# Performance work log

Hardware: AMD Instinct MI355X
Metric: run time of the kernel (lower is better)

Reference implementation:

```python
import jax, jax.numpy as jnp
import numpy as np

B, S, D, H, DK = 8, 1024, 1024, 16, 64
DV = D // H  # 64


def setup_inputs() -> dict:
    key = jax.random.key(0)
    ks = jax.random.split(key, 9)
    s = 1.0 / np.sqrt(D)
    return {
        "x": jax.random.normal(ks[0], (B, S, D), dtype=jnp.float32),
        "masks": jnp.ones((B, S), dtype=jnp.int32),
        "Wq": jax.random.normal(ks[1], (D, H * DK), dtype=jnp.float32) * s,
        "bq": jnp.zeros((H * DK,), dtype=jnp.float32),
        "Wk": jax.random.normal(ks[2], (D, H * DK), dtype=jnp.float32) * s,
        "bk": jnp.zeros((H * DK,), dtype=jnp.float32),
        "Wv": jax.random.normal(ks[3], (D, H * DV), dtype=jnp.float32) * s,
        "bv": jnp.zeros((H * DV,), dtype=jnp.float32),
        "Wo": jax.random.normal(ks[4], (H * DV, D), dtype=jnp.float32) * s,
        "bo": jnpp_zeros() if False else jnp.zeros((D,), dtype=jnp.float32),
    }


def reference(x, masks, Wq, bq, Wk, bk, Wv, bv, Wo, bo):
    # projections -> [B, H, S, d]
    q = (x @ Wq + bq).reshape(B, S, H, DK).transpose(0, 2, 1, 3)
    k = (x @ Wk + bk).reshape(B, S, H, DK).transpose(0, 2, 1, 3)
    v = (x @ Wv + bv).reshape(B, S, H, DV).transpose(0, 2, 1, 3)
    # scaled dot-product attention with padding mask
    logits = jnp.einsum('bhqd,bhkd->bhqk', q, k) / jnp.sqrt(jnp.float32(DK))
    mask = masks[:, None, None, :]  # [B,1,1,S]
    logits = jnp.where(mask == 0, jnp.float32(-1e9), logits)
    scores = jax.nn.softmax(logits, axis=-1)
    out = jnp.einsum('bhqk,bhkd->bhqd', scores, v)
    out = out.transpose(0, 2, 1, 3).reshape(B, S, H * DV)
    # output projection; dropout is identity in eval mode
    return out @ Wo + bo
```

## Files before the change

### kernel.cpp

```cpp
#include <hip/hip_runtime.h>
#include <stdint.h>

#define B_ 8
#define S_ 1024
#define D_ 1024
#define H_ 16
#define DK_ 64
#define DV_ 64

typedef __attribute__((ext_vector_type(8))) short short8;
typedef __attribute__((ext_vector_type(4))) float f32x4;

__device__ __forceinline__ unsigned short f2bf(float f) {
  union { float f; unsigned u; } v; v.f = f;
  return (unsigned short)((v.u + 0x7fffu + ((v.u >> 16) & 1u)) >> 16);
}
__device__ __forceinline__ unsigned short f2bf_trunc(float f) {
  union { float f; unsigned u; } v; v.f = f;
  return (unsigned short)(v.u >> 16);
}

__device__ __forceinline__ void ld_lds16(const unsigned short* g, unsigned short* l) {
  __builtin_amdgcn_global_load_lds((const __attribute__((address_space(1))) void*)g,
                                   (__attribute__((address_space(3))) void*)l, 16, 0, 0);
}

__global__ __launch_bounds__(256) void prep_kernel(const float* __restrict__ x,
                                                   unsigned short* __restrict__ xb,
                                                   const float* __restrict__ W0,
                                                   const float* __restrict__ W1,
                                                   const float* __restrict__ W2,
                                                   const float* __restrict__ W3,
                                                   unsigned short* __restrict__ T0,
                                                   unsigned short* __restrict__ T1,
                                                   unsigned short* __restrict__ T2,
                                                   unsigned short* __restrict__ T3) {
  const int z = blockIdx.z;
  if (z >= 4) {
    size_t blk = (size_t)(z - 4) * 256 + blockIdx.y * 16 + blockIdx.x;
    size_t i = (blk * 256 + threadIdx.x) * 4;
    float4 v = *(const float4*)(x + i);
    ushort4 o;
    o.x = f2bf(v.x); o.y = f2bf(v.y); o.z = f2bf(v.z); o.w = f2bf(v.w);
    *(ushort4*)(xb + i) = o;
    return;
  }
  __shared__ __align__(16) unsigned short tl[64][65];
  const float* W; unsigned short* Wt;
  switch (z) {
    case 0: W = W0; Wt = T0; break;
    case 1: W = W1; Wt = T1; break;
    case 2: W = W2; Wt = T2; break;
    default: W = W3; Wt = T3; break;
  }
  const int xx = threadIdx.x & 63;
  const int y4 = threadIdx.x >> 6;
  const int bn = blockIdx.x * 64;
  const int bk = blockIdx.y * 64;
  #pragma unroll
  for (int r = y4; r < 64; r += 4)
    tl[r][xx] = f2bf(W[(size_t)(bk + r) * 1024 + bn + xx]);
  __syncthreads();
  #pragma unroll
  for (int r = y4; r < 64; r += 4)
    Wt[(size_t)(bn + r) * 1024 + bk + xx] = tl[xx][r];
}


struct SJob { const unsigned short* g; unsigned short* l; };

__device__ __forceinline__ void stage128(const unsigned short* __restrict__ G,
                                         unsigned short* __restrict__ L, int t) {
  #pragma unroll
  for (int i = 0; i < 2; i++) {
    int s = i * 512 + t;
    int r = s >> 3, cb = s & 7;
    int c = cb ^ (r & 7);
    ld_lds16(G + (size_t)r * 1024 + c * 8, L + (size_t)s * 8);
  }
}

template <bool SW>
__device__ __forceinline__ f32x4 MM(short8 a, short8 b, f32x4 c) {
  if constexpr (SW) return __builtin_amdgcn_mfma_f32_16x16x32_bf16(b, a, c, 0, 0, 0);
  else              return __builtin_amdgcn_mfma_f32_16x16x32_bf16(a, b, c, 0, 0, 0);
}

template <bool SW, int VM>
__device__ __forceinline__ void ktile(const unsigned short* __restrict__ As_,
                                      const unsigned short* __restrict__ Bs_,
                                      f32x4 (&acc)[4][4],
                                      SJob s0, SJob s1, SJob s2,
                                      int t, int wm, int wn, int l15, int quad, int l7) {
  const int cb0 = (quad ^ l7) * 8;
  const int cb1 = ((4 | quad) ^ l7) * 8;
  short8 b0[4], b1[4];

  short8 a0k0 = *(const short8*)&As_[(wm + 0 * 16 + l15) * 64 + cb0];
  short8 a1k0 = *(const short8*)&As_[(wm + 1 * 16 + l15) * 64 + cb0];
  #pragma unroll
  for (int ni = 0; ni < 4; ni++)
    b0[ni] = *(const short8*)&Bs_[(wn + ni * 16 + l15) * 64 + cb0];
  if (s0.g) stage128(s0.g, s0.l, t);
  __builtin_amdgcn_s_barrier();
  asm volatile("s_waitcnt lgkmcnt(0)" ::: "memory");
  __builtin_amdgcn_s_setprio(1);
  #pragma unroll
  for (int ni = 0; ni < 4; ni++) {
    acc[0][ni] = MM<SW>(a0k0, b0[ni], acc[0][ni]);
    acc[1][ni] = MM<SW>(a1k0, b0[ni], acc[1][ni]);
  }
  __builtin_amdgcn_s_setprio(0);
  __builtin_amdgcn_s_barrier();

  short8 a0k1 = *(const short8*)&As_[(wm + 0 * 16 + l15) * 64 + cb1];
  short8 a1k1 = *(const short8*)&As_[(wm + 1 * 16 + l15) * 64 + cb1];
  #pragma unroll
  for (int ni = 0; ni < 4; ni++)
    b1[ni] = *(const short8*)&Bs_[(wn + ni * 16 + l15) * 64 + cb1];
  if (s1.g) stage128(s1.g, s1.l, t);
  __builtin_amdgcn_s_barrier();
  asm volatile("s_waitcnt lgkmcnt(0)" ::: "memory");
  __builtin_amdgcn_s_setprio(1);
  #pragma unroll
  for (int ni = 0; ni < 4; ni++) {
    acc[0][ni] = MM<SW>(a0k1, b1[ni], acc[0][ni]);
    acc[1][ni] = MM<SW>(a1k1, b1[ni], acc[1][ni]);
  }
  __builtin_amdgcn_s_setprio(0);
  __builtin_amdgcn_s_barrier();

  short8 a2k0 = *(const short8*)&As_[(wm + 2 * 16 + l15) * 64 + cb0];
  short8 a3k0 = *(const short8*)&As_[(wm + 3 * 16 + l15) * 64 + cb0];
  if (s2.g) stage128(s2.g, s2.l, t);
  __builtin_amdgcn_s_barrier();
  asm volatile("s_waitcnt lgkmcnt(0)" ::: "memory");
  __builtin_amdgcn_s_setprio(1);
  #pragma unroll
  for (int ni = 0; ni < 4; ni++) {
    acc[2][ni] = MM<SW>(a2k0, b0[ni], acc[2][ni]);
    acc[3][ni] = MM<SW>(a3k0, b0[ni], acc[3][ni]);
  }
  __builtin_amdgcn_s_setprio(0);
  __builtin_amdgcn_s_barrier();

  short8 a2k1 = *(const short8*)&As_[(wm + 2 * 16 + l15) * 64 + cb1];
  short8 a3k1 = *(const short8*)&As_[(wm + 3 * 16 + l15) * 64 + cb1];
  __builtin_amdgcn_s_barrier();
  asm volatile("s_waitcnt lgkmcnt(0)" ::: "memory");
  __builtin_amdgcn_s_setprio(1);
  #pragma unroll
  for (int ni = 0; ni < 4; ni++) {
    acc[2][ni] = MM<SW>(a2k1, b1[ni], acc[2][ni]);
    acc[3][ni] = MM<SW>(a3k1, b1[ni], acc[3][ni]);
  }
  __builtin_amdgcn_s_setprio(0);
  if constexpr (VM == 2) asm volatile("s_waitcnt vmcnt(2)" ::: "memory");
  else                   asm volatile("s_waitcnt vmcnt(0)" ::: "memory");
  __builtin_amdgcn_s_barrier();
}

template <bool SW>
__device__ __forceinline__ void gemm_core(const unsigned short* __restrict__ Ag,
                                          const unsigned short* __restrict__ Bg,
                                          unsigned short* __restrict__ Asl,
                                          unsigned short* __restrict__ Bsl,
                                          f32x4 (&acc)[4][4],
                                          int t, int wm, int wn, int l15, int quad, int l7) {
  stage128(Ag, &Asl[0], t);
  stage128(Ag + 128 * 1024, &Asl[8192], t);
  stage128(Bg, &Bsl[0], t);
  stage128(Bg + 64, &Bsl[8192], t);
  asm volatile("s_waitcnt vmcnt(2)" ::: "memory");
  __builtin_amdgcn_s_barrier();

  #pragma unroll 1
  for (int tt = 0; tt < 7; tt++) {
    const int J0 = 2 * tt;
    ktile<SW, 2>(&Asl[0], &Bsl[0], acc,
                 SJob{Ag + (size_t)(J0 + 1) * 64,              &Asl[16384]},
                 SJob{Ag + (size_t)(J0 + 1) * 64 + 128 * 1024, &Asl[16384 + 8192]},
                 SJob{Bg + (size_t)(J0 + 2) * 64,              &Bsl[0]},
                 t, wm, wn, l15, quad, l7);
    ktile<SW, 2>(&Asl[16384], &Bsl[8192], acc,
                 SJob{Ag + (size_t)(J0 + 2) * 64,              &Asl[0]},
                 SJob{Ag + (size_t)(J0 + 2) * 64 + 128 * 1024, &Asl[8192]},
                 SJob{Bg + (size_t)(J0 + 3) * 64,              &Bsl[8192]},
                 t, wm, wn, l15, quad, l7);
  }
  ktile<SW, 0>(&Asl[0], &Bsl[0], acc,
               SJob{Ag + (size_t)15 * 64,              &Asl[16384]},
               SJob{Ag + (size_t)15 * 64 + 128 * 1024, &Asl[16384 + 8192]},
               SJob{nullptr, nullptr},
               t, wm, wn, l15, quad, l7);
  ktile<SW, 0>(&Asl[16384], &Bsl[8192], acc,
               SJob{nullptr, nullptr}, SJob{nullptr, nullptr}, SJob{nullptr, nullptr},
               t, wm, wn, l15, quad, l7);
}

__global__ __launch_bounds__(512, 2) void gemm_qkv8(const unsigned short* __restrict__ A,
                                                    const unsigned short* __restrict__ Bt,
                                                    const float* __restrict__ bq,
                                                    const float* __restrict__ bk,
                                                    const float* __restrict__ bv,
                                                    const int* __restrict__ masks,
                                                    unsigned short* __restrict__ q,
                                                    unsigned short* __restrict__ kk,
                                                    unsigned short* __restrict__ vT) {
  extern __shared__ unsigned short lds[];
  unsigned short* Asl = lds;
  unsigned short* Bsl = lds + 2 * 16384;
  const int t = threadIdx.x;
  const int w = t >> 6, lane = t & 63;
  const int l15 = lane & 15, quad = lane >> 4, l7 = l15 & 7;
  const int bm = blockIdx.y * 256, bn = blockIdx.x * 128;
  const int wm = (w >> 1) * 64, wn = (w & 1) * 64;
  const bool vsec = (blockIdx.x >= 16);
  const unsigned short* Ag = A + (size_t)bm * 1024;
  const unsigned short* Bg = Bt + (size_t)bn * 1024;

  f32x4 acc[4][4] = {};
  if (!vsec) gemm_core<false>(Ag, Bg, Asl, Bsl, acc, t, wm, wn, l15, quad, l7);
  else       gemm_core<true >(Ag, Bg, Asl, Bsl, acc, t, wm, wn, l15, quad, l7);

  if (!vsec) {
    int sec = blockIdx.x >> 3;
    const float* bsel = (sec == 0) ? bq : bk;
    unsigned short* dst = (sec == 0) ? q : kk;
    float scale = (sec == 0) ? 0.180336880f : 1.0f;
    #pragma unroll
    for (int ni = 0; ni < 4; ni++) {
      int c = (bn & 1023) + wn + ni * 16 + l15;
      float bvv = bsel[c];
      int hh = c >> 6, d = c & 63;
      #pragma unroll
      for (int mi = 0; mi < 4; mi++) {
        int row0 = bm + wm + mi * 16 + quad * 4;
        #pragma unroll
        for (int r = 0; r < 4; r++) {
          int row = row0 + r;
          int b = row >> 10, s = row & 1023;
          dst[(((size_t)(b * H_ + hh)) * S_ + s) * DK_ + d] = f2bf((acc[mi][ni][r] + bvv) * scale);
        }
      }
    }
  } else {
    #pragma unroll
    for (int ni = 0; ni < 4; ni++) {
      int cbase = (bn & 1023) + wn + ni * 16;
      #pragma unroll
      for (int mi = 0; mi < 4; mi++) {
        int row = bm + wm + mi * 16 + l15;
        int b = row >> 10, s = row & 1023;
        float mf = (masks[b * S_ + s] != 0) ? 1.0f : 0.0f;
        #pragma unroll
        for (int r = 0; r < 4; r++) {
          int c = cbase + quad * 4 + r;
          int hh = c >> 6, d = c & 63;
          vT[(((size_t)(b * H_ + hh)) * DV_ + d) * S_ + s] = f2bf((acc[mi][ni][r] + bv[c]) * mf);
        }
      }
    }
  }
}

__global__ __launch_bounds__(512, 2) void gemm_out8(const unsigned short* __restrict__ A,
                                                    const unsigned short* __restrict__ Bt,
                                                    const float* __restrict__ bias,
                                                    float* __restrict__ Cout) {
  extern __shared__ unsigned short lds[];
  unsigned short* Asl = lds;
  unsigned short* Bsl = lds + 2 * 16384;
  const int t = threadIdx.x;
  const int w = t >> 6, lane = t & 63;
  const int l15 = lane & 15, quad = lane >> 4, l7 = l15 & 7;
  const int bm = blockIdx.y * 256, bn = blockIdx.x * 128;
  const int wm = (w >> 1) * 64, wn = (w & 1) * 64;
  const unsigned short* Ag = A + (size_t)bm * 1024;
  const unsigned short* Bg = Bt + (size_t)bn * 1024;

  f32x4 acc[4][4] = {};
  gemm_core<false>(Ag, Bg, Asl, Bsl, acc, t, wm, wn, l15, quad, l7);

  #pragma unroll
  for (int ni = 0; ni < 4; ni++) {
    int col = bn + wn + ni * 16 + l15;
    float bvv = bias[col];
    #pragma unroll
    for (int mi = 0; mi < 4; mi++) {
      int row0 = bm + wm + mi * 16 + quad * 4;
      #pragma unroll
      for (int r = 0; r < 4; r++)
        Cout[(size_t)(row0 + r) * 1024 + col] = acc[mi][ni][r] + bvv;
    }
  }
}

#define PLD 72
#define VROWS 65
__global__ __launch_bounds__(256) void attn_kernel(const unsigned short* __restrict__ Q,
                                                   const unsigned short* __restrict__ Kb,
                                                   const unsigned short* __restrict__ Vt,
                                                   const int* __restrict__ masks,
                                                   unsigned short* __restrict__ O) {
  __shared__ __align__(16) unsigned short Pl[128 * PLD];
  __shared__ __align__(16) unsigned short Ks[2 * 64 * 64];
  __shared__ __align__(16) unsigned short Vs[(2 * VROWS + 15) * 64];
  const int t = threadIdx.x;
  const int wave = t >> 6, lane = t & 63;
  const int l15 = lane & 15, quad = lane >> 4;
  const int l7 = l15 & 7;
  const int bh = blockIdx.x;
  const int qt = blockIdx.y;
  const int b = bh >> 4, h = bh & 15;

  const unsigned short* Qg = Q + ((size_t)bh * S_ + qt * 128) * DK_;
  const unsigned short* Kg = Kb + (size_t)bh * S_ * DK_;
  const unsigned short* Vg = Vt + (size_t)bh * DV_ * S_;
  const int wslot = (t & ~63);

  int mv[4];
  #pragma unroll
  for (int j = 0; j < 4; j++)
    mv[j] = masks[b * S_ + (j * 4 + wave) * 64 + lane];

  short8 aq[2][2];
  #pragma unroll
  for (int mb = 0; mb < 2; mb++)
    #pragma unroll
    for (int kf = 0; kf < 2; kf++)
      aq[mb][kf] = *(const short8*)(Qg + (size_t)(wave * 32 + mb * 16 + l15) * 64 + kf * 32 + quad * 8);

  auto stage = [&](int kt, int buf) {
    const unsigned short* Kt = Kg + (size_t)kt * 64 * DK_;
    unsigned short* Kd = &Ks[buf * 4096];
    unsigned short* Vd = &Vs[buf * (VROWS * 64)];
    #pragma unroll
    for (int i = 0; i < 2; i++) {
      int p = i * 256 + t;
      int rk = p >> 3, ck = (p & 7) ^ (rk & 7);
      ld_lds16(Kt + (size_t)rk * DK_ + ck * 8, &Kd[(i * 256 + wslot) * 8]);
      ld_lds16(Vg + (size_t)rk * S_ + kt * 64 + ck * 8, &Vd[(i * 256 + wslot) * 8]);
    }
    if (wave == (kt & 3))
      Vd[64 * 64 + lane] = (mv[kt >> 2] != 0) ? (unsigned short)0x3F80 : (unsigned short)0;
  };

  f32x4 o_acc[2][5] = {};

  stage(0, 0);
  __syncthreads();

  #pragma unroll 2
  for (int kt = 0; kt < 16; kt++) {
    const int cur = kt & 1;
    if (kt < 15) stage(kt + 1, cur ^ 1);
    const unsigned short* Kc = &Ks[cur * 4096];
    const unsigned short* Vc = &Vs[cur * (VROWS * 64)];

    f32x4 sc[2][4];
    #pragma unroll
    for (int n = 0; n < 4; n++) {
      short8 bk0 = *(const short8*)&Kc[(n * 16 + l15) * 64 + (quad ^ l7) * 8];
      short8 bk1 = *(const short8*)&Kc[(n * 16 + l15) * 64 + ((4 + quad) ^ l7) * 8];
      #pragma unroll
      for (int mb = 0; mb < 2; mb++) {
        f32x4 c = {};
        c = __builtin_amdgcn_mfma_f32_16x16x32_bf16(bk0, aq[mb][0], c, 0, 0, 0);
        c = __builtin_amdgcn_mfma_f32_16x16x32_bf16(bk1, aq[mb][1], c, 0, 0, 0);
        sc[mb][n] = c;
      }
    }
    #pragma unroll
    for (int mb = 0; mb < 2; mb++)
      #pragma unroll
      for (int n = 0; n < 4; n++) {
        ushort4 pk;
        pk.x = f2bf_trunc(__builtin_amdgcn_exp2f(sc[mb][n][0]));
        pk.y = f2bf_trunc(__builtin_amdgcn_exp2f(sc[mb][n][1]));
        pk.z = f2bf_trunc(__builtin_amdgcn_exp2f(sc[mb][n][2]));
        pk.w = f2bf_trunc(__builtin_amdgcn_exp2f(sc[mb][n][3]));
        *(ushort4*)&Pl[(wave * 32 + mb * 16 + l15) * PLD + n * 16 + quad * 4] = pk;
      }
    #pragma unroll
    for (int kf = 0; kf < 2; kf++) {
      short8 ap[2];
      #pragma unroll
      for (int mb = 0; mb < 2; mb++)
        ap[mb] = *(const short8*)&Pl[(wave * 32 + mb * 16 + l15) * PLD + kf * 32 + quad * 8];
      #pragma unroll
      for (int n = 0; n < 5; n++) {
        short8 bv = *(const short8*)&Vc[(n * 16 + l15) * 64 + ((kf * 4 + quad) ^ l7) * 8];
        #pragma unroll
        for (int mb = 0; mb < 2; mb++)
          o_acc[mb][n] = __builtin_amdgcn_mfma_f32_16x16x32_bf16(ap[mb], bv, o_acc[mb][n], 0, 0, 0);
      }
    }
    __syncthreads();
  }

  #pragma unroll
  for (int mb = 0; mb < 2; mb++)
    #pragma unroll
    for (int r = 0; r < 4; r++) {
      float l = __shfl(o_acc[mb][4][r], lane & 48, 64);
      float inv = __builtin_amdgcn_rcpf(l);
      int qrow = qt * 128 + wave * 32 + mb * 16 + quad * 4 + r;
      #pragma unroll
      for (int n = 0; n < 4; n++) {
        int col = h * 64 + n * 16 + l15;
        O[((size_t)b * S_ + qrow) * D_ + col] = f2bf(o_acc[mb][n][r] * inv);
      }
    }
}

extern "C" void kernel_launch(void* const* d_in, const int* in_sizes, int n_in,
                              void* d_out, int out_size, void* d_ws, size_t ws_size,
                              hipStream_t stream) {
  (void)in_sizes; (void)n_in; (void)out_size; (void)ws_size;
  const float* x  = (const float*)d_in[0];
  const int* masks = (const int*)d_in[1];
  const float* Wq = (const float*)d_in[2];
  const float* bq = (const float*)d_in[3];
  const float* Wk = (const float*)d_in[4];
  const float* bk = (const float*)d_in[5];
  const float* Wv = (const float*)d_in[6];
  const float* bv = (const float*)d_in[7];
  const float* Wo = (const float*)d_in[8];
  const float* bo = (const float*)d_in[9];

  char* p = (char*)d_ws;
  unsigned short* xb    = (unsigned short*)p; p += (size_t)8192 * 1024 * 2;
  unsigned short* WqkvT = (unsigned short*)p; p += (size_t)3072 * 1024 * 2;
  unsigned short* WoT   = (unsigned short*)p; p += (size_t)1024 * 1024 * 2;
  unsigned short* q     = (unsigned short*)p; p += (size_t)8192 * 1024 * 2;
  unsigned short* kk    = (unsigned short*)p; p += (size_t)8192 * 1024 * 2;
  unsigned short* vT    = (unsigned short*)p; p += (size_t)8192 * 1024 * 2;
  unsigned short* at    = (unsigned short*)p; p += (size_t)8192 * 1024 * 2;

  static bool attr_done = false;
  if (!attr_done) {
    hipFuncSetAttribute((const void*)gemm_qkv8, hipFuncAttributeMaxDynamicSharedMemorySize, 98304);
    hipFuncSetAttribute((const void*)gemm_out8, hipFuncAttributeMaxDynamicSharedMemorySize, 98304);
    attr_done = true;
  }

  prep_kernel<<<dim3(16, 16, 36), 256, 0, stream>>>(
      x, xb, Wq, Wk, Wv, Wo,
      WqkvT, WqkvT + (size_t)1024 * 1024, WqkvT + (size_t)2048 * 1024, WoT);
  gemm_qkv8<<<dim3(24, 32), 512, 98304, stream>>>(xb, WqkvT, bq, bk, bv, masks, q, kk, vT);
  attn_kernel<<<dim3(128, 8), 256, 0, stream>>>(q, kk, vT, masks, at);
  gemm_out8<<<dim3(8, 32), 512, 98304, stream>>>(at, WoT, bo, (float*)d_out);
}
```

Before: 239.3 us.

## Restructure GEMM k-tile into two phases with triple-buffered B staging

Replaces the four-phase k-tile loop body, which had several barriers per tile and interleaved A and B fragment loads, with a two-phase version. Each phase loads all four A and four B fragments and issues a full 4x4 block of MFMAs. All three global-to-LDS staging jobs are now issued up front in the first phase. B gets a third LDS buffer so it can be prefetched two tiles ahead, and the k-loop is unrolled by six to rotate the buffers. The aim is fewer barriers and more overlap between memory and MFMA work, at the cost of more LDS per block and higher register pressure from holding all fragments at once.

```diff
diff --git a/kernel.cpp b/kernel.cpp
--- a/kernel.cpp
+++ b/kernel.cpp
@@ -87,76 +87,54 @@
 }
 
 template <bool SW, int VM>
-__device__ __forceinline__ void ktile(const unsigned short* __restrict__ As_,
-                                      const unsigned short* __restrict__ Bs_,
-                                      f32x4 (&acc)[4][4],
-                                      SJob s0, SJob s1, SJob s2,
-                                      int t, int wm, int wn, int l15, int quad, int l7) {
+__device__ __forceinline__ void ktile2(const unsigned short* __restrict__ As_,
+                                       const unsigned short* __restrict__ Bs_,
+                                       f32x4 (&acc)[4][4],
+                                       SJob a0, SJob a1, SJob b2,
+                                       int t, int wm, int wn, int l15, int quad, int l7) {
   const int cb0 = (quad ^ l7) * 8;
   const int cb1 = ((4 | quad) ^ l7) * 8;
-  short8 b0[4], b1[4];
-
-  short8 a0k0 = *(const short8*)&As_[(wm + 0 * 16 + l15) * 64 + cb0];
-  short8 a1k0 = *(const short8*)&As_[(wm + 1 * 16 + l15) * 64 + cb0];
+  short8 af[4], bf[4];
+
+  #pragma unroll
+  for (int mi = 0; mi < 4; mi++)
+    af[mi] = *(const short8*)&As_[(wm + mi * 16 + l15) * 64 + cb0];
   #pragma unroll
   for (int ni = 0; ni < 4; ni++)
-    b0[ni] = *(const short8*)&Bs_[(wn + ni * 16 + l15) * 64 + cb0];
-  if (s0.g) stage128(s0.g, s0.l, t);
+    bf[ni] = *(const short8*)&Bs_[(wn + ni * 16 + l15) * 64 + cb0];
+  if (a0.g) stage128(a0.g, a0.l, t);
+  if (a1.g) stage128(a1.g, a1.l, t);
+  if (b2.g) stage128(b2.g, b2.l, t);
   __builtin_amdgcn_s_barrier();
   asm volatile("s_waitcnt lgkmcnt(0)" ::: "memory");
   __builtin_amdgcn_s_setprio(1);
   #pragma unroll
-  for (int ni = 0; ni < 4; ni++) {
-    acc[0][ni] = MM<SW>(a0k0, b0[ni], acc[0][ni]);
-    acc[1][ni] = MM<SW>(a1k0, b0[ni], acc[1][ni]);
-  }
+  for (int mi = 0; mi < 4; mi++)
+    #pragma unroll
+    for (int ni = 0; ni < 4; ni++)
+      acc[mi][ni] = MM<SW>(af[mi], bf[ni], acc[mi][ni]);
   __builtin_amdgcn_s_setprio(0);
   __builtin_amdgcn_s_barrier();
 
-  short8 a0k1 = *(const short8*)&As_[(wm + 0 * 16 + l15) * 64 + cb1];
-  short8 a1k1 = *(const short8*)&As_[(wm + 1 * 16 + l15) * 64 + cb1];
+  #pragma unroll
+  for (int mi = 0; mi < 4; mi++)
+    af[mi] = *(const short8*)&As_[(wm + mi * 16 + l15) * 64 + cb1];
   #pragma unroll
   for (int ni = 0; ni < 4; ni++)
-    b1[ni] = *(const short8*)&Bs_[(wn + ni * 16 + l15) * 64 + cb1];
-  if (s1.g) stage128(s1.g, s1.l, t);
+    bf[ni] = *(const short8*)&Bs_[(wn + ni * 16 + l15) * 64 + cb1];
   __builtin_amdgcn_s_barrier();
   asm volatile("s_waitcnt lgkmcnt(0)" ::: "memory");
   __builtin_amdgcn_s_setprio(1);
   #pragma unroll
-  for (int ni = 0; ni < 4; ni++) {
-    acc[0][ni] = MM<SW>(a0k1, b1[ni], acc[0][ni]);
-    acc[1][ni] = MM<SW>(a1k1, b1[ni], acc[1][ni]);
-  }
+  for (int mi = 0; mi < 4; mi++)
+    #pragma unroll
+    for (int ni = 0; ni < 4; ni++)
+      acc[mi][ni] = MM<SW>(af[mi], bf[ni], acc[mi][ni]);
   __builtin_amdgcn_s_setprio(0);
-  __builtin_amdgcn_s_barrier();
-
-  short8 a2k0 = *(const short8*)&As_[(wm + 2 * 16 + l15) * 64 + cb0];
-  short8 a3k0 = *(const short8*)&As_[(wm + 3 * 16 + l15) * 64 + cb0];
-  if (s2.g) stage128(s2.g, s2.l, t);
-  __builtin_amdgcn_s_barrier();
-  asm volatile("s_waitcnt lgkmcnt(0)" ::: "memory");
-  __builtin_amdgcn_s_setprio(1);
-  #pragma unroll
-  for (int ni = 0; ni < 4; ni++) {
-    acc[2][ni] = MM<SW>(a2k0, b0[ni], acc[2][ni]);
-    acc[3][ni] = MM<SW>(a3k0, b0[ni], acc[3][ni]);
-  }
-  __builtin_amdgcn_s_setprio(0);
-  __builtin_amdgcn_s_barrier();
-
-  short8 a2k1 = *(const short8*)&As_[(wm + 2 * 16 + l15) * 64 + cb1];
-  short8 a3k1 = *(const short8*)&As_[(wm + 3 * 16 + l15) * 64 + cb1];
-  __builtin_amdgcn_s_barrier();
-  asm volatile("s_waitcnt lgkmcnt(0)" ::: "memory");
-  __builtin_amdgcn_s_setprio(1);
-  #pragma unroll
-  for (int ni = 0; ni < 4; ni++) {
-    acc[2][ni] = MM<SW>(a2k1, b1[ni], acc[2][ni]);
-    acc[3][ni] = MM<SW>(a3k1, b1[ni], acc[3][ni]);
-  }
-  __builtin_amdgcn_s_setprio(0);
-  if constexpr (VM == 2) asm volatile("s_waitcnt vmcnt(2)" ::: "memory");
-  else                   asm volatile("s_waitcnt vmcnt(0)" ::: "memory");
+  if constexpr (VM >= 0) {
+    if constexpr (VM == 2) asm volatile("s_waitcnt vmcnt(2)" ::: "memory");
+    else                   asm volatile("s_waitcnt vmcnt(0)" ::: "memory");
+  }
   __builtin_amdgcn_s_barrier();
 }
 
@@ -175,27 +153,40 @@
   __builtin_amdgcn_s_barrier();
 
   #pragma unroll 1
-  for (int tt = 0; tt < 7; tt++) {
-    const int J0 = 2 * tt;
-    ktile<SW, 2>(&Asl[0], &Bsl[0], acc,
-                 SJob{Ag + (size_t)(J0 + 1) * 64,              &Asl[16384]},
-                 SJob{Ag + (size_t)(J0 + 1) * 64 + 128 * 1024, &Asl[16384 + 8192]},
-                 SJob{Bg + (size_t)(J0 + 2) * 64,              &Bsl[0]},
+  for (int Jb = 0; Jb < 12; Jb += 6) {
+    const unsigned short* Agj = Ag + (size_t)Jb * 64;
+    const unsigned short* Bgj = Bg + (size_t)Jb * 64;
+    ktile2<SW, 2>(&Asl[0], &Bsl[0], acc,
+                  SJob{Agj + 64, &Asl[16384]}, SJob{Agj + 64 + 128 * 1024, &Asl[16384 + 8192]},
+                  SJob{Bgj + 128, &Bsl[16384]}, t, wm, wn, l15, quad, l7);
+    ktile2<SW, 2>(&Asl[16384], &Bsl[8192], acc,
+                  SJob{Agj + 128, &Asl[0]}, SJob{Agj + 128 + 128 * 1024, &Asl[8192]},
+                  SJob{Bgj + 192, &Bsl[0]}, t, wm, wn, l15, quad, l7);
+    ktile2<SW, 2>(&Asl[0], &Bsl[16384], acc,
+                  SJob{Agj + 192, &Asl[16384]}, SJob{Agj + 192 + 128 * 1024, &Asl[16384 + 8192]},
+                  SJob{Bgj + 256, &Bsl[8192]}, t, wm, wn, l15, quad, l7);
+    ktile2<SW, 2>(&Asl[16384], &Bsl[0], acc,
+                  SJob{Agj + 256, &Asl[0]}, SJob{Agj + 256 + 128 * 1024, &Asl[8192]},
+                  SJob{Bgj + 320, &Bsl[16384]}, t, wm, wn, l15, quad, l7);
+    ktile2<SW, 2>(&Asl[0], &Bsl[8192], acc,
+                  SJob{Agj + 320, &Asl[16384]}, SJob{Agj + 320 + 128 * 1024, &Asl[16384 + 8192]},
+                  SJob{Bgj + 384, &Bsl[0]}, t, wm, wn, l15, quad, l7);
+    ktile2<SW, 2>(&Asl[16384], &Bsl[16384], acc,
+                  SJob{Agj + 384, &Asl[0]}, SJob{Agj + 384 + 128 * 1024, &Asl[8192]},
+                  SJob{Bgj + 448, &Bsl[8192]}, t, wm, wn, l15, quad, l7);
+  }
+  ktile2<SW, 2>(&Asl[0], &Bsl[0], acc,
+                SJob{Ag + 13 * 64, &Asl[16384]}, SJob{Ag + 13 * 64 + 128 * 1024, &Asl[16384 + 8192]},
+                SJob{Bg + 14 * 64, &Bsl[16384]}, t, wm, wn, l15, quad, l7);
+  ktile2<SW, 2>(&Asl[16384], &Bsl[8192], acc,
+                SJob{Ag + 14 * 64, &Asl[0]}, SJob{Ag + 14 * 64 + 128 * 1024, &Asl[8192]},
+                SJob{Bg + 15 * 64, &Bsl[0]}, t, wm, wn, l15, quad, l7);
+  ktile2<SW, 0>(&Asl[0], &Bsl[16384], acc,
+                SJob{Ag + 15 * 64, &Asl[16384]}, SJob{Ag + 15 * 64 + 128 * 1024, &Asl[16384 + 8192]},
+                SJob{nullptr, nullptr}, t, wm, wn, l15, quad, l7);
+  ktile2<SW, -1>(&Asl[16384], &Bsl[0], acc,
+                 SJob{nullptr, nullptr}, SJob{nullptr, nullptr}, SJob{nullptr, nullptr},
                  t, wm, wn, l15, quad, l7);
-    ktile<SW, 2>(&Asl[16384], &Bsl[8192], acc,
-                 SJob{Ag + (size_t)(J0 + 2) * 64,              &Asl[0]},
-                 SJob{Ag + (size_t)(J0 + 2) * 64 + 128 * 1024, &Asl[8192]},
-                 SJob{Bg + (size_t)(J0 + 3) * 64,              &Bsl[8192]},
-                 t, wm, wn, l15, quad, l7);
-  }
-  ktile<SW, 0>(&Asl[0], &Bsl[0], acc,
-               SJob{Ag + (size_t)15 * 64,              &Asl[16384]},
-               SJob{Ag + (size_t)15 * 64 + 128 * 1024, &Asl[16384 + 8192]},
-               SJob{nullptr, nullptr},
-               t, wm, wn, l15, quad, l7);
-  ktile<SW, 0>(&Asl[16384], &Bsl[8192], acc,
-               SJob{nullptr, nullptr}, SJob{nullptr, nullptr}, SJob{nullptr, nullptr},
-               t, wm, wn, l15, quad, l7);
 }
 
 __global__ __launch_bounds__(512, 2) void gemm_qkv8(const unsigned short* __restrict__ A,
@@ -440,15 +431,15 @@
 
   static bool attr_done = false;
   if (!attr_done) {
-    hipFuncSetAttribute((const void*)gemm_qkv8, hipFuncAttributeMaxDynamicSharedMemorySize, 98304);
-    hipFuncSetAttribute((const void*)gemm_out8, hipFuncAttributeMaxDynamicSharedMemorySize, 98304);
+    hipFuncSetAttribute((const void*)gemm_qkv8, hipFuncAttributeMaxDynamicSharedMemorySize, 114688);
+    hipFuncSetAttribute((const void*)gemm_out8, hipFuncAttributeMaxDynamicSharedMemorySize, 114688);
     attr_done = true;
   }
 
   prep_kernel<<<dim3(16, 16, 36), 256, 0, stream>>>(
       x, xb, Wq, Wk, Wv, Wo,
       WqkvT, WqkvT + (size_t)1024 * 1024, WqkvT + (size_t)2048 * 1024, WoT);
-  gemm_qkv8<<<dim3(24, 32), 512, 98304, stream>>>(xb, WqkvT, bq, bk, bv, masks, q, kk, vT);
+  gemm_qkv8<<<dim3(24, 32), 512, 114688, stream>>>(xb, WqkvT, bq, bk, bv, masks, q, kk, vT);
   attn_kernel<<<dim3(128, 8), 256, 0, stream>>>(q, kk, vT, masks, at);
-  gemm_out8<<<dim3(8, 32), 512, 98304, stream>>>(at, WoT, bo, (float*)d_out);
-}
+  gemm_out8<<<dim3(8, 32), 512, 114688, stream>>>(at, WoT, bo, (float*)d_out);
+}
```

New measurement: 251.2 us. 1.05x slower.

## Shrink GEMM block tile to 128x128 with four waves and smaller LDS

Applied to the files above, without the earlier changes.

Both projection GEMMs move from 256x128 tiles with 8 waves (512 threads, 96KB LDS) to 128x128 tiles with 4 waves (256 threads, 64KB LDS), doubling the grid. Staging now uses 256 threads with four 16-byte loads each, and the pipeline's vmcnt waits and buffer layout are adjusted to match. The aim is more blocks for better CU fill, especially for the output GEMM, which previously had only 256 blocks. The cost is less reuse of B per block, which raises global and L2 traffic.

```diff
diff --git a/kernel.cpp b/kernel.cpp
--- a/kernel.cpp
+++ b/kernel.cpp
@@ -69,11 +69,11 @@
 
 struct SJob { const unsigned short* g; unsigned short* l; };
 
-__device__ __forceinline__ void stage128(const unsigned short* __restrict__ G,
-                                         unsigned short* __restrict__ L, int t) {
-  #pragma unroll
-  for (int i = 0; i < 2; i++) {
-    int s = i * 512 + t;
+__device__ __forceinline__ void stage_t256(const unsigned short* __restrict__ G,
+                                           unsigned short* __restrict__ L, int t) {
+  #pragma unroll
+  for (int i = 0; i < 4; i++) {
+    int s = i * 256 + t;
     int r = s >> 3, cb = s & 7;
     int c = cb ^ (r & 7);
     ld_lds16(G + (size_t)r * 1024 + c * 8, L + (size_t)s * 8);
@@ -87,118 +87,116 @@
 }
 
 template <bool SW, int VM>
-__device__ __forceinline__ void ktile(const unsigned short* __restrict__ As_,
-                                      const unsigned short* __restrict__ Bs_,
-                                      f32x4 (&acc)[4][4],
-                                      SJob s0, SJob s1, SJob s2,
-                                      int t, int wm, int wn, int l15, int quad, int l7) {
+__device__ __forceinline__ void ktile128(const unsigned short* __restrict__ As_,
+                                         const unsigned short* __restrict__ Bs_,
+                                         f32x4 (&acc)[4][4],
+                                         SJob sA, SJob sB,
+                                         int t, int wm, int wn, int l15, int quad, int l7) {
   const int cb0 = (quad ^ l7) * 8;
   const int cb1 = ((4 | quad) ^ l7) * 8;
-  short8 b0[4], b1[4];
-
-  short8 a0k0 = *(const short8*)&As_[(wm + 0 * 16 + l15) * 64 + cb0];
-  short8 a1k0 = *(const short8*)&As_[(wm + 1 * 16 + l15) * 64 + cb0];
+  short8 b0[4], b1[4], a0, a1;
+
   #pragma unroll
   for (int ni = 0; ni < 4; ni++)
     b0[ni] = *(const short8*)&Bs_[(wn + ni * 16 + l15) * 64 + cb0];
-  if (s0.g) stage128(s0.g, s0.l, t);
+  a0 = *(const short8*)&As_[(wm + 0 * 16 + l15) * 64 + cb0];
+  a1 = *(const short8*)&As_[(wm + 1 * 16 + l15) * 64 + cb0];
+  if (sA.g) stage_t256(sA.g, sA.l, t);
   __builtin_amdgcn_s_barrier();
   asm volatile("s_waitcnt lgkmcnt(0)" ::: "memory");
   __builtin_amdgcn_s_setprio(1);
   #pragma unroll
   for (int ni = 0; ni < 4; ni++) {
-    acc[0][ni] = MM<SW>(a0k0, b0[ni], acc[0][ni]);
-    acc[1][ni] = MM<SW>(a1k0, b0[ni], acc[1][ni]);
+    acc[0][ni] = MM<SW>(a0, b0[ni], acc[0][ni]);
+    acc[1][ni] = MM<SW>(a1, b0[ni], acc[1][ni]);
   }
   __builtin_amdgcn_s_setprio(0);
   __builtin_amdgcn_s_barrier();
 
-  short8 a0k1 = *(const short8*)&As_[(wm + 0 * 16 + l15) * 64 + cb1];
-  short8 a1k1 = *(const short8*)&As_[(wm + 1 * 16 + l15) * 64 + cb1];
   #pragma unroll
   for (int ni = 0; ni < 4; ni++)
     b1[ni] = *(const short8*)&Bs_[(wn + ni * 16 + l15) * 64 + cb1];
-  if (s1.g) stage128(s1.g, s1.l, t);
+  a0 = *(const short8*)&As_[(wm + 0 * 16 + l15) * 64 + cb1];
+  a1 = *(const short8*)&As_[(wm + 1 * 16 + l15) * 64 + cb1];
   __builtin_amdgcn_s_barrier();
   asm volatile("s_waitcnt lgkmcnt(0)" ::: "memory");
   __builtin_amdgcn_s_setprio(1);
   #pragma unroll
   for (int ni = 0; ni < 4; ni++) {
-    acc[0][ni] = MM<SW>(a0k1, b1[ni], acc[0][ni]);
-    acc[1][ni] = MM<SW>(a1k1, b1[ni], acc[1][ni]);
+    acc[0][ni] = MM<SW>(a0, b1[ni], acc[0][ni]);
+    acc[1][ni] = MM<SW>(a1, b1[ni], acc[1][ni]);
   }
   __builtin_amdgcn_s_setprio(0);
   __builtin_amdgcn_s_barrier();
 
-  short8 a2k0 = *(const short8*)&As_[(wm + 2 * 16 + l15) * 64 + cb0];
-  short8 a3k0 = *(const short8*)&As_[(wm + 3 * 16 + l15) * 64 + cb0];
-  if (s2.g) stage128(s2.g, s2.l, t);
+  a0 = *(const short8*)&As_[(wm + 2 * 16 + l15) * 64 + cb0];
+  a1 = *(const short8*)&As_[(wm + 3 * 16 + l15) * 64 + cb0];
+  if (sB.g) stage_t256(sB.g, sB.l, t);
   __builtin_amdgcn_s_barrier();
   asm volatile("s_waitcnt lgkmcnt(0)" ::: "memory");
   __builtin_amdgcn_s_setprio(1);
   #pragma unroll
   for (int ni = 0; ni < 4; ni++) {
-    acc[2][ni] = MM<SW>(a2k0, b0[ni], acc[2][ni]);
-    acc[3][ni] = MM<SW>(a3k0, b0[ni], acc[3][ni]);
+    acc[2][ni] = MM<SW>(a0, b0[ni], acc[2][ni]);
+    acc[3][ni] = MM<SW>(a1, b0[ni], acc[3][ni]);
   }
   __builtin_amdgcn_s_setprio(0);
   __builtin_amdgcn_s_barrier();
 
-  short8 a2k1 = *(const short8*)&As_[(wm + 2 * 16 + l15) * 64 + cb1];
-  short8 a3k1 = *(const short8*)&As_[(wm + 3 * 16 + l15) * 64 + cb1];
+  a0 = *(const short8*)&As_[(wm + 2 * 16 + l15) * 64 + cb1];
+  a1 = *(const short8*)&As_[(wm + 3 * 16 + l15) * 64 + cb1];
   __builtin_amdgcn_s_barrier();
   asm volatile("s_waitcnt lgkmcnt(0)" ::: "memory");
   __builtin_amdgcn_s_setprio(1);
   #pragma unroll
   for (int ni = 0; ni < 4; ni++) {
-    acc[2][ni] = MM<SW>(a2k1, b1[ni], acc[2][ni]);
-    acc[3][ni] = MM<SW>(a3k1, b1[ni], acc[3][ni]);
+    acc[2][ni] = MM<SW>(a0, b1[ni], acc[2][ni]);
+    acc[3][ni] = MM<SW>(a1, b1[ni], acc[3][ni]);
   }
   __builtin_amdgcn_s_setprio(0);
-  if constexpr (VM == 2) asm volatile("s_waitcnt vmcnt(2)" ::: "memory");
-  else                   asm volatile("s_waitcnt vmcnt(0)" ::: "memory");
+  if constexpr (VM == 4) asm volatile("s_waitcnt vmcnt(4)" ::: "memory");
+  if constexpr (VM == 0) asm volatile("s_waitcnt vmcnt(0)" ::: "memory");
   __builtin_amdgcn_s_barrier();
 }
 
 template <bool SW>
-__device__ __forceinline__ void gemm_core(const unsigned short* __restrict__ Ag,
-                                          const unsigned short* __restrict__ Bg,
-                                          unsigned short* __restrict__ Asl,
-                                          unsigned short* __restrict__ Bsl,
-                                          f32x4 (&acc)[4][4],
-                                          int t, int wm, int wn, int l15, int quad, int l7) {
-  stage128(Ag, &Asl[0], t);
-  stage128(Ag + 128 * 1024, &Asl[8192], t);
-  stage128(Bg, &Bsl[0], t);
-  stage128(Bg + 64, &Bsl[8192], t);
-  asm volatile("s_waitcnt vmcnt(2)" ::: "memory");
+__device__ __forceinline__ void gemm_core128(const unsigned short* __restrict__ Ag,
+                                             const unsigned short* __restrict__ Bg,
+                                             unsigned short* __restrict__ Asl,
+                                             unsigned short* __restrict__ Bsl,
+                                             f32x4 (&acc)[4][4],
+                                             int t, int wm, int wn, int l15, int quad, int l7) {
+  unsigned short* A0 = Asl;
+  unsigned short* A1 = Asl + 8192;
+  unsigned short* B0 = Bsl;
+  unsigned short* B1 = Bsl + 8192;
+
+  stage_t256(Ag,      A0, t);
+  stage_t256(Bg,      B0, t);
+  stage_t256(Bg + 64, B1, t);
+  asm volatile("s_waitcnt vmcnt(4)" ::: "memory");
   __builtin_amdgcn_s_barrier();
 
   #pragma unroll 1
-  for (int tt = 0; tt < 7; tt++) {
-    const int J0 = 2 * tt;
-    ktile<SW, 2>(&Asl[0], &Bsl[0], acc,
-                 SJob{Ag + (size_t)(J0 + 1) * 64,              &Asl[16384]},
-                 SJob{Ag + (size_t)(J0 + 1) * 64 + 128 * 1024, &Asl[16384 + 8192]},
-                 SJob{Bg + (size_t)(J0 + 2) * 64,              &Bsl[0]},
-                 t, wm, wn, l15, quad, l7);
-    ktile<SW, 2>(&Asl[16384], &Bsl[8192], acc,
-                 SJob{Ag + (size_t)(J0 + 2) * 64,              &Asl[0]},
-                 SJob{Ag + (size_t)(J0 + 2) * 64 + 128 * 1024, &Asl[8192]},
-                 SJob{Bg + (size_t)(J0 + 3) * 64,              &Bsl[8192]},
-                 t, wm, wn, l15, quad, l7);
-  }
-  ktile<SW, 0>(&Asl[0], &Bsl[0], acc,
-               SJob{Ag + (size_t)15 * 64,              &Asl[16384]},
-               SJob{Ag + (size_t)15 * 64 + 128 * 1024, &Asl[16384 + 8192]},
-               SJob{nullptr, nullptr},
-               t, wm, wn, l15, quad, l7);
-  ktile<SW, 0>(&Asl[16384], &Bsl[8192], acc,
-               SJob{nullptr, nullptr}, SJob{nullptr, nullptr}, SJob{nullptr, nullptr},
-               t, wm, wn, l15, quad, l7);
-}
-
-__global__ __launch_bounds__(512, 2) void gemm_qkv8(const unsigned short* __restrict__ A,
+  for (int J = 0; J < 14; J += 2) {
+    ktile128<SW, 4>(A0, B0, acc,
+                    SJob{Ag + (size_t)(J + 1) * 64, A1},
+                    SJob{Bg + (size_t)(J + 2) * 64, B0},
+                    t, wm, wn, l15, quad, l7);
+    ktile128<SW, 4>(A1, B1, acc,
+                    SJob{Ag + (size_t)(J + 2) * 64, A0},
+                    SJob{Bg + (size_t)(J + 3) * 64, B1},
+                    t, wm, wn, l15, quad, l7);
+  }
+  ktile128<SW, 0>(A0, B0, acc,
+                  SJob{Ag + (size_t)15 * 64, A1}, SJob{nullptr, nullptr},
+                  t, wm, wn, l15, quad, l7);
+  ktile128<SW, -1>(A1, B1, acc,
+                   SJob{nullptr, nullptr}, SJob{nullptr, nullptr},
+                   t, wm, wn, l15, quad, l7);
+}
+
+__global__ __launch_bounds__(256, 2) void gemm_qkv8(const unsigned short* __restrict__ A,
                                                     const unsigned short* __restrict__ Bt,
                                                     const float* __restrict__ bq,
                                                     const float* __restrict__ bk,
@@ -209,19 +207,19 @@
                                                     unsigned short* __restrict__ vT) {
   extern __shared__ unsigned short lds[];
   unsigned short* Asl = lds;
-  unsigned short* Bsl = lds + 2 * 16384;
+  unsigned short* Bsl = lds + 16384;
   const int t = threadIdx.x;
-  const int w = t >> 6, lane = t & 63;
+  const int wave = t >> 6, lane = t & 63;
   const int l15 = lane & 15, quad = lane >> 4, l7 = l15 & 7;
-  const int bm = blockIdx.y * 256, bn = blockIdx.x * 128;
-  const int wm = (w >> 1) * 64, wn = (w & 1) * 64;
+  const int bm = blockIdx.y * 128, bn = blockIdx.x * 128;
+  const int wm = (wave & 1) * 64, wn = (wave >> 1) * 64;
   const bool vsec = (blockIdx.x >= 16);
   const unsigned short* Ag = A + (size_t)bm * 1024;
   const unsigned short* Bg = Bt + (size_t)bn * 1024;
 
   f32x4 acc[4][4] = {};
-  if (!vsec) gemm_core<false>(Ag, Bg, Asl, Bsl, acc, t, wm, wn, l15, quad, l7);
-  else       gemm_core<true >(Ag, Bg, Asl, Bsl, acc, t, wm, wn, l15, quad, l7);
+  if (!vsec) gemm_core128<false>(Ag, Bg, Asl, Bsl, acc, t, wm, wn, l15, quad, l7);
+  else       gemm_core128<true >(Ag, Bg, Asl, Bsl, acc, t, wm, wn, l15, quad, l7);
 
   if (!vsec) {
     int sec = blockIdx.x >> 3;
@@ -264,23 +262,23 @@
   }
 }
 
-__global__ __launch_bounds__(512, 2) void gemm_out8(const unsigned short* __restrict__ A,
+__global__ __launch_bounds__(256, 2) void gemm_out8(const unsigned short* __restrict__ A,
                                                     const unsigned short* __restrict__ Bt,
                                                     const float* __restrict__ bias,
                                                     float* __restrict__ Cout) {
   extern __shared__ unsigned short lds[];
   unsigned short* Asl = lds;
-  unsigned short* Bsl = lds + 2 * 16384;
+  unsigned short* Bsl = lds + 16384;
   const int t = threadIdx.x;
-  const int w = t >> 6, lane = t & 63;
+  const int wave = t >> 6, lane = t & 63;
   const int l15 = lane & 15, quad = lane >> 4, l7 = l15 & 7;
-  const int bm = blockIdx.y * 256, bn = blockIdx.x * 128;
-  const int wm = (w >> 1) * 64, wn = (w & 1) * 64;
+  const int bm = blockIdx.y * 128, bn = blockIdx.x * 128;
+  const int wm = (wave & 1) * 64, wn = (wave >> 1) * 64;
   const unsigned short* Ag = A + (size_t)bm * 1024;
   const unsigned short* Bg = Bt + (size_t)bn * 1024;
 
   f32x4 acc[4][4] = {};
-  gemm_core<false>(Ag, Bg, Asl, Bsl, acc, t, wm, wn, l15, quad, l7);
+  gemm_core128<false>(Ag, Bg, Asl, Bsl, acc, t, wm, wn, l15, quad, l7);
 
   #pragma unroll
   for (int ni = 0; ni < 4; ni++) {
@@ -440,15 +438,15 @@
 
   static bool attr_done = false;
   if (!attr_done) {
-    hipFuncSetAttribute((const void*)gemm_qkv8, hipFuncAttributeMaxDynamicSharedMemorySize, 98304);
-    hipFuncSetAttribute((const void*)gemm_out8, hipFuncAttributeMaxDynamicSharedMemorySize, 98304);
+    hipFuncSetAttribute((const void*)gemm_qkv8, hipFuncAttributeMaxDynamicSharedMemorySize, 65536);
+    hipFuncSetAttribute((const void*)gemm_out8, hipFuncAttributeMaxDynamicSharedMemorySize, 65536);
     attr_done = true;
   }
 
   prep_kernel<<<dim3(16, 16, 36), 256, 0, stream>>>(
       x, xb, Wq, Wk, Wv, Wo,
       WqkvT, WqkvT + (size_t)1024 * 1024, WqkvT + (size_t)2048 * 1024, WoT);
-  gemm_qkv8<<<dim3(24, 32), 512, 98304, stream>>>(xb, WqkvT, bq, bk, bv, masks, q, kk, vT);
+  gemm_qkv8<<<dim3(24, 64), 256, 65536, stream>>>(xb, WqkvT, bq, bk, bv, masks, q, kk, vT);
   attn_kernel<<<dim3(128, 8), 256, 0, stream>>>(q, kk, vT, masks, at);
-  gemm_out8<<<dim3(8, 32), 512, 98304, stream>>>(at, WoT, bo, (float*)d_out);
-}
+  gemm_out8<<<dim3(8, 64), 256, 65536, stream>>>(at, WoT, bo, (float*)d_out);
+}
```

New measurement: 241.8 us. About the same (+1.1%).
